# Kernel tuning notes

Hardware: AMD Instinct MI355X
Metric: run time of the kernel (lower is better)

## Reference

```python
import jax, jax.numpy as jnp
import numpy as np


def _lstm_cell(x, h, c, W_ih, W_hh, b_ih, b_hh):
    # torch gate order: input, forget, cell(g), output
    g = x @ W_ih.T + h @ W_hh.T + b_ih + b_hh
    i, f, gg, o = jnp.split(g, 4, axis=-1)
    c_new = jax.nn.sigmoid(f) * c + jax.nn.sigmoid(i) * jnp.tanh(gg)
    h_new = jax.nn.sigmoid(o) * jnp.tanh(c_new)
    return h_new, c_new


def setup_inputs() -> dict:
    key = jax.random.key(0)
    ks = jax.random.split(key, 11)
    T, B, D, E, H, V = 64, 4096, 32, 32, 5, 10
    IN = D + 3 * E  # 128 = input_size
    s = 0.1
    return {
        "horizon": T,
        "hidden": jax.random.normal(ks[0], (2, B, H), jnp.float32),
        "cell": jax.random.normal(ks[1], (2, B, H), jnp.float32),
        "dec_x": jax.random.normal(ks[2], (T, B, D), jnp.float32),
        "mote_id_cat": jax.random.randint(ks[3], (T, B), 0, V),
        "fault_type_cat": jax.random.randint(ks[4], (T, B), 0, V),
        "mote_fault_cat": jax.random.randint(ks[5], (T, B), 0, V),
        "mote_embed": jax.random.normal(ks[6], (V, E), jnp.float32),
        "W_ih0": jax.random.normal(ks[7], (4 * H, IN), jnp.float32) * s,
        "W_hh0": jax.random.normal(ks[8], (4 * H, H), jnp.float32) * s,
        "b_ih0": jnp.zeros((4 * H,), jnp.float32),
        "b_hh0": jnp.zeros((4 * H,), jnp.float32),
        "W_ih1": jax.random.normal(ks[9], (4 * H, H), jnp.float32) * s,
        "W_hh1": jax.random.normal(ks[10], (4 * H, H), jnp.float32) * s,
        "b_ih1": jnp.zeros((4 * H,), jnp.float32),
        "b_hh1": jnp.zeros((4 * H,), jnp.float32),
    }


def reference(horizon, hidden, cell, dec_x, mote_id_cat, fault_type_cat,
              mote_fault_cat, mote_embed, W_ih0, W_hh0, b_ih0, b_hh0,
              W_ih1, W_hh1, b_ih1, b_hh1):
    # Faithful to source: ALL three categorical features use mote_embed.
    e1 = mote_embed[mote_id_cat]      # [T,B,E]
    e2 = mote_embed[fault_type_cat]   # [T,B,E]
    e3 = mote_embed[mote_fault_cat]   # [T,B,E]
    x = jnp.concatenate([dec_x, e1, e2, e3], axis=-1)[:horizon]  # [T,B,IN]

    # Source re-feeds the SAME initial (hidden, cell) at every horizon step,
    # so steps are independent -> vmap over time (no carried recurrence).
    def step(xt):  # xt: [B, IN]
        h1, _ = _lstm_cell(xt, hidden[0], cell[0], W_ih0, W_hh0, b_ih0, b_hh0)
        h2, _ = _lstm_cell(h1, hidden[1], cell[1], W_ih1, W_hh1, b_ih1, b_hh1)
        return h2  # top-layer output, [B, H]

    return jax.vmap(step)(x)  # [T, B, H]
```

## Files before the change

kernel.cpp:

```cpp
#include <hip/hip_runtime.h>
#include <math.h>

#define HDIM 5
#define GATES 20
#define DDIM 32
#define EDIM 32
#define INDIM 128
#define VOC 10

__device__ __forceinline__ float sigmoidf_(float x) {
    return __builtin_amdgcn_rcpf(1.0f + __expf(-x));
}
__device__ __forceinline__ float tanhf_(float x) {
    float e = __expf(-2.0f * x);
    return fmaf(2.0f, __builtin_amdgcn_rcpf(1.0f + e), -1.0f);
}

__global__ __launch_bounds__(256) void decoder_kernel(
    const float* __restrict__ hidden,
    const float* __restrict__ cell,
    const float* __restrict__ dec_x,
    const int*   __restrict__ mid_cat,
    const int*   __restrict__ ft_cat,
    const int*   __restrict__ mf_cat,
    const float* __restrict__ emb,
    const float* __restrict__ W_ih0,
    const float* __restrict__ W_hh0,
    const float* __restrict__ b_ih0,
    const float* __restrict__ b_hh0,
    const float* __restrict__ W_ih1,
    const float* __restrict__ W_hh1,
    const float* __restrict__ b_ih1,
    const float* __restrict__ b_hh1,
    float* __restrict__ out,
    int B, int total)
{
    __shared__ float sP[3][VOC][GATES];

    const int tid = threadIdx.x;
    for (int j = tid; j < 3 * VOC * GATES; j += 256) {
        int s = j / (VOC * GATES);
        int rem = j % (VOC * GATES);
        int v = rem / GATES, r = rem % GATES;
        const float* ev = emb + v * EDIM;
        const float* wv = W_ih0 + r * INDIM + DDIM + s * EDIM;
        float a = 0.0f;
        #pragma unroll
        for (int e = 0; e < EDIM; ++e) a = fmaf(ev[e], wv[e], a);
        sP[s][v][r] = a;
    }
    __syncthreads();

    const int idx = blockIdx.x * 256 + tid;
    if (idx >= total) return;
    const int t = idx / B;
    const int b = idx - t * B;
    (void)t;

    float acc[GATES];
    {
        float hid0[HDIM];
        #pragma unroll
        for (int h = 0; h < HDIM; ++h) hid0[h] = hidden[(size_t)b * HDIM + h];
        #pragma unroll
        for (int r = 0; r < GATES; ++r) {
            float a = b_ih0[r] + b_hh0[r];
            #pragma unroll
            for (int h = 0; h < HDIM; ++h)
                a = fmaf(hid0[h], W_hh0[r * HDIM + h], a);
            acc[r] = a;
        }
        int vm = mid_cat[idx], vf = ft_cat[idx], vmf = mf_cat[idx];
        const float4* P0 = (const float4*)sP[0][vm];
        const float4* P1 = (const float4*)sP[1][vf];
        const float4* P2 = (const float4*)sP[2][vmf];
        #pragma unroll
        for (int k = 0; k < 5; ++k) {
            float4 p0 = P0[k], p1 = P1[k], p2 = P2[k];
            acc[4 * k + 0] += p0.x + p1.x + p2.x;
            acc[4 * k + 1] += p0.y + p1.y + p2.y;
            acc[4 * k + 2] += p0.z + p1.z + p2.z;
            acc[4 * k + 3] += p0.w + p1.w + p2.w;
        }
    }

    {
        const float4* xp = (const float4*)dec_x + (size_t)idx * (DDIM / 4);
        float4 x[DDIM / 4];
        #pragma unroll
        for (int c4 = 0; c4 < DDIM / 4; ++c4) x[c4] = xp[c4];
        #pragma unroll
        for (int r = 0; r < GATES; ++r) {
            const float* w = W_ih0 + r * INDIM;
            float a = acc[r];
            #pragma unroll
            for (int c4 = 0; c4 < DDIM / 4; ++c4) {
                a = fmaf(x[c4].x, w[4 * c4 + 0], a);
                a = fmaf(x[c4].y, w[4 * c4 + 1], a);
                a = fmaf(x[c4].z, w[4 * c4 + 2], a);
                a = fmaf(x[c4].w, w[4 * c4 + 3], a);
            }
            acc[r] = a;
        }
    }

    float h1[HDIM];
    #pragma unroll
    for (int r = 0; r < HDIM; ++r) {
        float c0 = cell[(size_t)b * HDIM + r];
        float ii = sigmoidf_(acc[r]);
        float ff = sigmoidf_(acc[HDIM + r]);
        float gg = tanhf_(acc[2 * HDIM + r]);
        float oo = sigmoidf_(acc[3 * HDIM + r]);
        float cn = fmaf(ff, c0, ii * gg);
        h1[r] = oo * tanhf_(cn);
    }

    float g1[GATES];
    {
        float hid1[HDIM];
        #pragma unroll
        for (int h = 0; h < HDIM; ++h) hid1[h] = hidden[((size_t)B + b) * HDIM + h];
        #pragma unroll
        for (int r = 0; r < GATES; ++r) {
            float a = b_ih1[r] + b_hh1[r];
            #pragma unroll
            for (int h = 0; h < HDIM; ++h) {
                a = fmaf(hid1[h], W_hh1[r * HDIM + h], a);
                a = fmaf(h1[h],   W_ih1[r * HDIM + h], a);
            }
            g1[r] = a;
        }
    }

    #pragma unroll
    for (int r = 0; r < HDIM; ++r) {
        float c1 = cell[((size_t)B + b) * HDIM + r];
        float ii = sigmoidf_(g1[r]);
        float ff = sigmoidf_(g1[HDIM + r]);
        float gg = tanhf_(g1[2 * HDIM + r]);
        float oo = sigmoidf_(g1[3 * HDIM + r]);
        float cn = fmaf(ff, c1, ii * gg);
        out[(size_t)idx * HDIM + r] = oo * tanhf_(cn);
    }
}

extern "C" void kernel_launch(void* const* d_in, const int* in_sizes, int n_in,
                              void* d_out, int out_size, void* d_ws, size_t ws_size,
                              hipStream_t stream) {
    const float* hidden = (const float*)d_in[1];
    const float* cellp  = (const float*)d_in[2];
    const float* dec_x  = (const float*)d_in[3];
    const int*   midc   = (const int*)d_in[4];
    const int*   ftc    = (const int*)d_in[5];
    const int*   mfc    = (const int*)d_in[6];
    const float* emb    = (const float*)d_in[7];
    const float* W_ih0  = (const float*)d_in[8];
    const float* W_hh0  = (const float*)d_in[9];
    const float* b_ih0  = (const float*)d_in[10];
    const float* b_hh0  = (const float*)d_in[11];
    const float* W_ih1  = (const float*)d_in[12];
    const float* W_hh1  = (const float*)d_in[13];
    const float* b_ih1  = (const float*)d_in[14];
    const float* b_hh1  = (const float*)d_in[15];
    float* out = (float*)d_out;

    int B = in_sizes[1] / (2 * HDIM);
    int horizon = out_size / (B * HDIM);
    int total = horizon * B;
    int grid = (total + 255) / 256;
    if (grid < 1) grid = 1;

    decoder_kernel<<<grid, 256, 0, stream>>>(
        hidden, cellp, dec_x, midc, ftc, mfc, emb,
        W_ih0, W_hh0, b_ih0, b_hh0, W_ih1, W_hh1, b_ih1, b_hh1,
        out, B, total);
}
```

Baseline: 126.0 us.

## Precompute time-invariant hidden-state gate terms and embedding projections in a prologue kernel

Adds a precompute kernel that computes, once, the embedding-projection table and the per-batch recurrent gate contributions (W_hh·h plus biases) for both layers, storing them in workspace. The main kernel then loads these instead of recomputing them for every timestep and block, and uses launch_bounds hinting for occupancy. This removes redundant per-block table builds and per-timestep hidden-state matmuls, at the cost of an extra launch and extra workspace reads (80 floats per batch element per thread).

```diff
diff --git a/kernel.cpp b/kernel.cpp
--- a/kernel.cpp
+++ b/kernel.cpp
@@ -7,6 +7,8 @@
 #define EDIM 32
 #define INDIM 128
 #define VOC 10
+#define SPN (3 * VOC * GATES)
+#define HH_OFF 1024
 
 __device__ __forceinline__ float sigmoidf_(float x) {
     return __builtin_amdgcn_rcpf(1.0f + __expf(-x));
@@ -16,92 +18,116 @@
     return fmaf(2.0f, __builtin_amdgcn_rcpf(1.0f + e), -1.0f);
 }
 
-__global__ __launch_bounds__(256) void decoder_kernel(
+__global__ __launch_bounds__(256) void precompute_kernel(
     const float* __restrict__ hidden,
+    const float* __restrict__ emb,
+    const float* __restrict__ W_ih0,
+    const float* __restrict__ W_hh0, const float* __restrict__ b_ih0,
+    const float* __restrict__ b_hh0,
+    const float* __restrict__ W_hh1, const float* __restrict__ b_ih1,
+    const float* __restrict__ b_hh1,
+    float* __restrict__ ws, int B)
+{
+    int gid = blockIdx.x * 256 + threadIdx.x;
+    if (gid < SPN) {
+        int s = gid / (VOC * GATES);
+        int rem = gid % (VOC * GATES);
+        int v = rem / GATES, r = rem % GATES;
+        const float4* ev = (const float4*)(emb + v * EDIM);
+        const float4* wv = (const float4*)(W_ih0 + r * INDIM + DDIM + s * EDIM);
+        float a = 0.0f;
+        #pragma unroll
+        for (int k = 0; k < EDIM / 4; ++k) {
+            float4 e4 = ev[k], w4 = wv[k];
+            a = fmaf(e4.x, w4.x, a); a = fmaf(e4.y, w4.y, a);
+            a = fmaf(e4.z, w4.z, a); a = fmaf(e4.w, w4.w, a);
+        }
+        ws[gid] = a;
+    }
+    if (gid < B) {
+        float h0[HDIM], h1v[HDIM];
+        #pragma unroll
+        for (int h = 0; h < HDIM; ++h) {
+            h0[h]  = hidden[(size_t)gid * HDIM + h];
+            h1v[h] = hidden[((size_t)B + gid) * HDIM + h];
+        }
+        #pragma unroll
+        for (int r = 0; r < GATES; ++r) {
+            float a0 = b_ih0[r] + b_hh0[r];
+            float a1 = b_ih1[r] + b_hh1[r];
+            #pragma unroll
+            for (int h = 0; h < HDIM; ++h) {
+                a0 = fmaf(h0[h],  W_hh0[r * HDIM + h], a0);
+                a1 = fmaf(h1v[h], W_hh1[r * HDIM + h], a1);
+            }
+            ws[HH_OFF + (size_t)gid * GATES + r] = a0;
+            ws[HH_OFF + (size_t)(B + gid) * GATES + r] = a1;
+        }
+    }
+}
+
+__global__ __launch_bounds__(256, 4) void decoder_kernel(
     const float* __restrict__ cell,
     const float* __restrict__ dec_x,
-    const int*   __restrict__ mid_cat,
-    const int*   __restrict__ ft_cat,
-    const int*   __restrict__ mf_cat,
-    const float* __restrict__ emb,
+    const int*   __restrict__ midc,
+    const int*   __restrict__ ftc,
+    const int*   __restrict__ mfc,
     const float* __restrict__ W_ih0,
-    const float* __restrict__ W_hh0,
-    const float* __restrict__ b_ih0,
-    const float* __restrict__ b_hh0,
     const float* __restrict__ W_ih1,
-    const float* __restrict__ W_hh1,
-    const float* __restrict__ b_ih1,
-    const float* __restrict__ b_hh1,
+    const float* __restrict__ ws,
     float* __restrict__ out,
     int B, int total)
 {
-    __shared__ float sP[3][VOC][GATES];
-
-    const int tid = threadIdx.x;
-    for (int j = tid; j < 3 * VOC * GATES; j += 256) {
-        int s = j / (VOC * GATES);
-        int rem = j % (VOC * GATES);
-        int v = rem / GATES, r = rem % GATES;
-        const float* ev = emb + v * EDIM;
-        const float* wv = W_ih0 + r * INDIM + DDIM + s * EDIM;
-        float a = 0.0f;
-        #pragma unroll
-        for (int e = 0; e < EDIM; ++e) a = fmaf(ev[e], wv[e], a);
-        sP[s][v][r] = a;
-    }
+    __shared__ float sP[SPN];
+    for (int j = threadIdx.x; j < SPN; j += 256) sP[j] = ws[j];
     __syncthreads();
 
-    const int idx = blockIdx.x * 256 + tid;
+    const int idx = blockIdx.x * 256 + threadIdx.x;
     if (idx >= total) return;
     const int t = idx / B;
     const int b = idx - t * B;
     (void)t;
 
+    const float4* xp = (const float4*)dec_x + (size_t)idx * (DDIM / 4);
+    float4 x[DDIM / 4];
+    #pragma unroll
+    for (int k = 0; k < DDIM / 4; ++k) x[k] = xp[k];
+
+    const int vm = midc[idx], vf = ftc[idx], vmf = mfc[idx];
+
     float acc[GATES];
-    {
-        float hid0[HDIM];
-        #pragma unroll
-        for (int h = 0; h < HDIM; ++h) hid0[h] = hidden[(size_t)b * HDIM + h];
-        #pragma unroll
-        for (int r = 0; r < GATES; ++r) {
-            float a = b_ih0[r] + b_hh0[r];
-            #pragma unroll
-            for (int h = 0; h < HDIM; ++h)
-                a = fmaf(hid0[h], W_hh0[r * HDIM + h], a);
-            acc[r] = a;
-        }
-        int vm = mid_cat[idx], vf = ft_cat[idx], vmf = mf_cat[idx];
-        const float4* P0 = (const float4*)sP[0][vm];
-        const float4* P1 = (const float4*)sP[1][vf];
-        const float4* P2 = (const float4*)sP[2][vmf];
-        #pragma unroll
-        for (int k = 0; k < 5; ++k) {
-            float4 p0 = P0[k], p1 = P1[k], p2 = P2[k];
-            acc[4 * k + 0] += p0.x + p1.x + p2.x;
-            acc[4 * k + 1] += p0.y + p1.y + p2.y;
-            acc[4 * k + 2] += p0.z + p1.z + p2.z;
-            acc[4 * k + 3] += p0.w + p1.w + p2.w;
-        }
-    }
-
-    {
-        const float4* xp = (const float4*)dec_x + (size_t)idx * (DDIM / 4);
-        float4 x[DDIM / 4];
-        #pragma unroll
-        for (int c4 = 0; c4 < DDIM / 4; ++c4) x[c4] = xp[c4];
-        #pragma unroll
-        for (int r = 0; r < GATES; ++r) {
-            const float* w = W_ih0 + r * INDIM;
-            float a = acc[r];
-            #pragma unroll
-            for (int c4 = 0; c4 < DDIM / 4; ++c4) {
-                a = fmaf(x[c4].x, w[4 * c4 + 0], a);
-                a = fmaf(x[c4].y, w[4 * c4 + 1], a);
-                a = fmaf(x[c4].z, w[4 * c4 + 2], a);
-                a = fmaf(x[c4].w, w[4 * c4 + 3], a);
-            }
-            acc[r] = a;
-        }
+    const float4* hh0p = (const float4*)(ws + HH_OFF + (size_t)b * GATES);
+    #pragma unroll
+    for (int k = 0; k < 5; ++k) {
+        float4 h4 = hh0p[k];
+        acc[4 * k + 0] = h4.x; acc[4 * k + 1] = h4.y;
+        acc[4 * k + 2] = h4.z; acc[4 * k + 3] = h4.w;
+    }
+
+    const float4* P0 = (const float4*)(sP + vm * GATES);
+    const float4* P1 = (const float4*)(sP + VOC * GATES + vf * GATES);
+    const float4* P2 = (const float4*)(sP + 2 * VOC * GATES + vmf * GATES);
+    #pragma unroll
+    for (int k = 0; k < 5; ++k) {
+        float4 p0 = P0[k], p1 = P1[k], p2 = P2[k];
+        acc[4 * k + 0] += p0.x + p1.x + p2.x;
+        acc[4 * k + 1] += p0.y + p1.y + p2.y;
+        acc[4 * k + 2] += p0.z + p1.z + p2.z;
+        acc[4 * k + 3] += p0.w + p1.w + p2.w;
+    }
+
+    #pragma unroll
+    for (int r = 0; r < GATES; ++r) {
+        const float* w = W_ih0 + r * INDIM;
+        float a = acc[r];
+        #pragma unroll
+        for (int k = 0; k < DDIM / 4; ++k) {
+            a = fmaf(x[k].x, w[4 * k + 0], a);
+            a = fmaf(x[k].y, w[4 * k + 1], a);
+            a = fmaf(x[k].z, w[4 * k + 2], a);
+            a = fmaf(x[k].w, w[4 * k + 3], a);
+        }
+        acc[r] = a;
     }
 
     float h1[HDIM];
@@ -117,20 +143,20 @@
     }
 
     float g1[GATES];
-    {
-        float hid1[HDIM];
-        #pragma unroll
-        for (int h = 0; h < HDIM; ++h) hid1[h] = hidden[((size_t)B + b) * HDIM + h];
-        #pragma unroll
-        for (int r = 0; r < GATES; ++r) {
-            float a = b_ih1[r] + b_hh1[r];
-            #pragma unroll
-            for (int h = 0; h < HDIM; ++h) {
-                a = fmaf(hid1[h], W_hh1[r * HDIM + h], a);
-                a = fmaf(h1[h],   W_ih1[r * HDIM + h], a);
-            }
-            g1[r] = a;
-        }
+    const float4* hh1p = (const float4*)(ws + HH_OFF + (size_t)(B + b) * GATES);
+    #pragma unroll
+    for (int k = 0; k < 5; ++k) {
+        float4 h4 = hh1p[k];
+        g1[4 * k + 0] = h4.x; g1[4 * k + 1] = h4.y;
+        g1[4 * k + 2] = h4.z; g1[4 * k + 3] = h4.w;
+    }
+    #pragma unroll
+    for (int r = 0; r < GATES; ++r) {
+        float a = g1[r];
+        #pragma unroll
+        for (int h = 0; h < HDIM; ++h)
+            a = fmaf(h1[h], W_ih1[r * HDIM + h], a);
+        g1[r] = a;
     }
 
     #pragma unroll
@@ -164,15 +190,19 @@
     const float* b_ih1  = (const float*)d_in[14];
     const float* b_hh1  = (const float*)d_in[15];
     float* out = (float*)d_out;
+    float* ws  = (float*)d_ws;
 
     int B = in_sizes[1] / (2 * HDIM);
     int horizon = out_size / (B * HDIM);
     int total = horizon * B;
+
+    int pre_n = (B > SPN ? B : SPN);
+    int pre_grid = (pre_n + 255) / 256;
+    precompute_kernel<<<pre_grid, 256, 0, stream>>>(
+        hidden, emb, W_ih0, W_hh0, b_ih0, b_hh0, W_hh1, b_ih1, b_hh1, ws, B);
+
     int grid = (total + 255) / 256;
     if (grid < 1) grid = 1;
-
     decoder_kernel<<<grid, 256, 0, stream>>>(
-        hidden, cellp, dec_x, midc, ftc, mfc, emb,
-        W_ih0, W_hh0, b_ih0, b_hh0, W_ih1, W_hh1, b_ih1, b_hh1,
-        out, B, total);
-}
+        cellp, dec_x, midc, ftc, mfc, W_ih0, W_ih1, ws, out, B, total);
+}
```

Result: faster. 119.2 us (-5.4%).
